# Kernel tuning notes

Measured on AMD Instinct MI355X. Metric: run time of the kernel, lower is better.

## Reference

```python
import jax, jax.numpy as jnp
import numpy as np

D_CONV = 4  # matches Mamba(d_conv=4)


def _silu(v):
    return v * jax.nn.sigmoid(v)


def _mamba_block(x, in_w, cw, cb, xw, dtw, dtb, A_log, Dp, ow):
    # x: (B, L, d_model)
    B, L, _ = x.shape
    d_inner, d_state = A_log.shape
    xz = x @ in_w.T                        # (B, L, 2*d_inner)
    xr, z = jnp.split(xz, 2, axis=-1)      # each (B, L, d_inner)
    # causal depthwise conv1d (pad d_conv-1 on the left, truncate to L)
    xp = jnp.pad(xr, ((0, 0), (D_CONV - 1, 0), (0, 0)))
    xc = sum(xp[:, k:k + L, :] * cw[:, k] for k in range(D_CONV)) + cb
    xc = _silu(xc)                         # (B, L, d_inner)
    dbl = xc @ xw.T                        # (B, L, dt_rank + 2*d_state)
    dt_rank = dbl.shape[-1] - 2 * d_state
    dt, Bm, Cm = jnp.split(dbl, [dt_rank, dt_rank + d_state], axis=-1)
    dt = jax.nn.softplus(dt @ dtw.T + dtb)  # (B, L, d_inner)
    A = -jnp.exp(A_log)                    # (d_inner, d_state)
    dA = jnp.exp(dt[..., None] * A)                          # (B, L, d_inner, d_state)
    dBx = dt[..., None] * Bm[:, :, None, :] * xc[..., None]  # (B, L, d_inner, d_state)

    def step(h, inputs):
        dA_t, dBx_t, C_t = inputs          # (B,d,s), (B,d,s), (B,s)
        h = dA_t * h + dBx_t
        y = jnp.einsum('bds,bs->bd', h, C_t)
        return h, y

    h0 = jnp.zeros((B, d_inner, d_state), x.dtype)
    _, ys = jax.lax.scan(step, h0, (dA.transpose(1, 0, 2, 3),
                                    dBx.transpose(1, 0, 2, 3),
                                    Cm.transpose(1, 0, 2)))
    y = ys.transpose(1, 0, 2) + xc * Dp    # skip term D*u
    y = y * _silu(z)                       # gated
    return y @ ow.T                        # (B, L, d_model)


def setup_inputs() -> dict:
    key = jax.random.key(0)
    d_model, d_state, n_layer = 1024, 16, 2
    d_inner = 2 * d_model
    dt_rank = d_model // 16  # ceil(1024/16)
    Bsz, L = 2, 1024
    ks = jax.random.split(key, 8)
    s = 0.02
    x = jax.random.normal(ks[0], (Bsz, L, d_model), jnp.float32)
    in_proj_w = jax.random.normal(ks[1], (n_layer, 2 * d_inner, d_model), jnp.float32) * s
    conv_w = jax.random.normal(ks[2], (n_layer, d_inner, D_CONV), jnp.float32) * 0.2
    conv_b = jnp.zeros((n_layer, d_inner), jnp.float32)
    x_proj_w = jax.random.normal(ks[3], (n_layer, dt_rank + 2 * d_state, d_inner), jnp.float32) * s
    dt_proj_w = jax.random.normal(ks[4], (n_layer, d_inner, dt_rank), jnp.float32) * s
    dt_proj_b = jax.random.uniform(ks[5], (n_layer, d_inner), jnp.float32, -5.0, -3.0)
    A_log = jnp.log(jnp.tile(jnp.arange(1, d_state + 1, dtype=jnp.float32), (n_layer, d_inner, 1)))
    D = jnp.ones((n_layer, d_inner), jnp.float32)
    out_proj_w = jax.random.normal(ks[6], (n_layer, d_model, d_inner), jnp.float32) * s
    return {"x": x, "in_proj_w": in_proj_w, "conv_w": conv_w, "conv_b": conv_b,
            "x_proj_w": x_proj_w, "dt_proj_w": dt_proj_w, "dt_proj_b": dt_proj_b,
            "A_log": A_log, "D": D, "out_proj_w": out_proj_w}


def reference(x, in_proj_w, conv_w, conv_b, x_proj_w, dt_proj_w, dt_proj_b, A_log, D, out_proj_w):
    n_layer = in_proj_w.shape[0]
    for i in range(n_layer):
        x = _mamba_block(x, in_proj_w[i], conv_w[i], conv_b[i], x_proj_w[i],
                         dt_proj_w[i], dt_proj_b[i], A_log[i], D[i], out_proj_w[i])
    return x
```

## Files before the change

kernel.cpp:

```cpp
#include <hip/hip_runtime.h>
#include <hip/hip_bf16.h>
#include <cmath>

typedef __bf16 bf16x8_t __attribute__((ext_vector_type(8)));
typedef float  f32x4_t  __attribute__((ext_vector_type(4)));
using bf16 = __hip_bfloat16;

#define LOG2E 1.44269504088896340736f
#define LN2   0.69314718055994530942f

#define AS1C(p) ((const __attribute__((address_space(1))) void*)(p))
#define AS3C(p) ((__attribute__((address_space(3))) void*)(p))

__device__ __forceinline__ float fexp2(float x) { return __builtin_amdgcn_exp2f(x); }
__device__ __forceinline__ float flog2(float x) { return __builtin_amdgcn_logf(x); }
__device__ __forceinline__ float frcp (float x) { return __builtin_amdgcn_rcpf(x); }

__global__ __launch_bounds__(256)
void cast_multi(const float* s0, bf16* d0, int e0,
                const float* s1, bf16* d1, int e1,
                const float* s2, bf16* d2, int e2,
                const float* s3, bf16* d3, int e3,
                const float* s4, bf16* d4, int e4)
{
    const int blk = blockIdx.x;
    const float* src; bf16* dst; int base;
    if      (blk < e0) { src = s0; dst = d0; base = blk; }
    else if (blk < e1) { src = s1; dst = d1; base = blk - e0; }
    else if (blk < e2) { src = s2; dst = d2; base = blk - e1; }
    else if (blk < e3) { src = s3; dst = d3; base = blk - e2; }
    else               { src = s4; dst = d4; base = blk - e3; }

    const int i = base * 256 + threadIdx.x;
    const float4* s = (const float4*)(src + (size_t)i * 8);
    float4 a = s[0], b = s[1];
    bf16 o[8];
    o[0] = __float2bfloat16(a.x); o[1] = __float2bfloat16(a.y);
    o[2] = __float2bfloat16(a.z); o[3] = __float2bfloat16(a.w);
    o[4] = __float2bfloat16(b.x); o[5] = __float2bfloat16(b.y);
    o[6] = __float2bfloat16(b.z); o[7] = __float2bfloat16(b.w);
    *(int4*)(dst + (size_t)i * 8) = *(int4*)o;
}

template<int MODE, bool SPLITK>
__global__ __launch_bounds__(256)
void gemm_bf16(const bf16* __restrict__ A, const bf16* __restrict__ B,
               float* __restrict__ Cf, bf16* __restrict__ Cb,
               int M, int N, int K, int lda, int ldb, int ldc)
{
    __shared__ __align__(16) bf16 At[2][64][32];
    __shared__ __align__(16) bf16 Bt[2][128][32];

    const int tid  = threadIdx.x;
    const int lane = tid & 63;
    const int wid  = tid >> 6;
    const int wr2  = wid & 1;
    const int wc2  = wid >> 1;
    const int fr   = lane & 15;
    const int fq   = lane >> 4;

    const int row0 = blockIdx.y * 64;
    const int col0 = blockIdx.x * 128;
    const int kb   = SPLITK ? blockIdx.z * K : 0;

    const int gA_row = wid * 16 + (lane >> 2);
    const int gB_row = wid * 32 + (lane >> 2);
    const int g_kp   = (((lane & 3) ^ ((lane >> 3) & 3)) * 8);
    const bf16* aP0 = A + (size_t)(row0 + gA_row) * lda + g_kp + kb;
    int bR0 = col0 + gB_row;      if (bR0 >= N) bR0 = N - 1;
    int bR1 = col0 + gB_row + 16; if (bR1 >= N) bR1 = N - 1;
    const bf16* bP0 = B + (size_t)bR0 * ldb + g_kp + kb;
    const bf16* bP1 = B + (size_t)bR1 * ldb + g_kp + kb;

    const int rchunk = (fq ^ ((fr >> 1) & 3)) * 8;

    f32x4_t acc[2][4];
    #pragma unroll
    for (int m = 0; m < 2; ++m)
        #pragma unroll
        for (int n = 0; n < 4; ++n)
            acc[m][n] = f32x4_t{0.f, 0.f, 0.f, 0.f};

    auto STAGE = [&](int buf, int k0) {
        __builtin_amdgcn_global_load_lds(AS1C(aP0 + k0), AS3C(&At[buf][wid * 16][0]),      16, 0, 0);
        __builtin_amdgcn_global_load_lds(AS1C(bP0 + k0), AS3C(&Bt[buf][wid * 32][0]),      16, 0, 0);
        __builtin_amdgcn_global_load_lds(AS1C(bP1 + k0), AS3C(&Bt[buf][wid * 32 + 16][0]), 16, 0, 0);
    };

    STAGE(0, 0);
    __syncthreads();
    int cur = 0;
    for (int k0 = 0; k0 < K; k0 += 32) {
        if (k0 + 32 < K) STAGE(cur ^ 1, k0 + 32);

        bf16x8_t af[2], bg[4];
        #pragma unroll
        for (int m = 0; m < 2; ++m)
            af[m] = *(const bf16x8_t*)&At[cur][wr2 * 32 + m * 16 + fr][rchunk];
        #pragma unroll
        for (int n = 0; n < 4; ++n)
            bg[n] = *(const bf16x8_t*)&Bt[cur][wc2 * 64 + n * 16 + fr][rchunk];
        #pragma unroll
        for (int m = 0; m < 2; ++m)
            #pragma unroll
            for (int n = 0; n < 4; ++n)
                acc[m][n] = __builtin_amdgcn_mfma_f32_16x16x32_bf16(
                    af[m], bg[n], acc[m][n], 0, 0, 0);

        __syncthreads();
        cur ^= 1;
    }

    float* Cfz = SPLITK ? (Cf + (size_t)blockIdx.z * M * ldc) : Cf;

    #pragma unroll
    for (int m = 0; m < 2; ++m) {
        #pragma unroll
        for (int n = 0; n < 4; ++n) {
            const int c = col0 + wc2 * 64 + n * 16 + fr;
            if (c < N) {
                #pragma unroll
                for (int r = 0; r < 4; ++r) {
                    const int rr = row0 + wr2 * 32 + m * 16 + fq * 4 + r;
                    if (SPLITK || MODE != 1) Cfz[(size_t)rr * ldc + c] = acc[m][n][r];
                    if (!SPLITK && MODE != 0) Cb[(size_t)rr * ldc + c] = __float2bfloat16(acc[m][n][r]);
                }
            }
        }
    }
}

__global__ __launch_bounds__(256)
void reduce_pk(const float* __restrict__ part, float* __restrict__ of,
               bf16* __restrict__ oh, int n4, int stride4, int S)
{
    const int i = blockIdx.x * blockDim.x + threadIdx.x;
    if (i >= n4) return;
    const float4* p4 = (const float4*)part;
    float4 s = p4[i];
    for (int k = 1; k < S; ++k) {
        float4 v = p4[(size_t)k * stride4 + i];
        s.x += v.x; s.y += v.y; s.z += v.z; s.w += v.w;
    }
    if (of) ((float4*)of)[i] = s;
    if (oh) {
        bf16 o[4];
        o[0] = __float2bfloat16(s.x); o[1] = __float2bfloat16(s.y);
        o[2] = __float2bfloat16(s.z); o[3] = __float2bfloat16(s.w);
        *(int2*)(oh + (size_t)i * 4) = *(int2*)o;
    }
}

__global__ __launch_bounds__(256)
void conv_silu(const bf16* __restrict__ xz, const float* __restrict__ cw,
               const float* __restrict__ cb, bf16* __restrict__ xc,
               int Bsz, int L, int dinner)
{
    const int nv = dinner / 4;
    const int L4 = L / 4;
    const int g  = blockIdx.x * blockDim.x + threadIdx.x;
    const int d4 = (g % nv) * 4;
    const int t4 = (g / nv) % L4;
    const int b  = g / (nv * L4);
    if (b >= Bsz) return;

    const int t0 = t4 * 4;
    const int ldxz = 2 * dinner;

    float4 w0 = *(const float4*)(cw + (size_t)(d4 + 0) * 4);
    float4 w1 = *(const float4*)(cw + (size_t)(d4 + 1) * 4);
    float4 w2 = *(const float4*)(cw + (size_t)(d4 + 2) * 4);
    float4 w3 = *(const float4*)(cw + (size_t)(d4 + 3) * 4);
    float4 bias = *(const float4*)(cb + d4);

    float4 r[7];
    const bf16* base = xz + (size_t)b * L * ldxz + d4;
    #pragma unroll
    for (int k = 0; k < 7; ++k) {
        const int ts = t0 - 3 + k;
        if (ts >= 0 && ts < L) {
            const bf16* rp = base + (size_t)ts * ldxz;
            r[k] = make_float4(__bfloat162float(rp[0]), __bfloat162float(rp[1]),
                               __bfloat162float(rp[2]), __bfloat162float(rp[3]));
        } else {
            r[k] = make_float4(0.f, 0.f, 0.f, 0.f);
        }
    }

    bf16* outp = xc + ((size_t)b * L + t0) * dinner + d4;
    #pragma unroll
    for (int j = 0; j < 4; ++j) {
        float4 acc = bias;
        #pragma unroll
        for (int k = 0; k < 4; ++k) {
            const float4 v = r[j + k];
            acc.x = fmaf(v.x, (&w0.x)[k], acc.x);
            acc.y = fmaf(v.y, (&w1.x)[k], acc.y);
            acc.z = fmaf(v.z, (&w2.x)[k], acc.z);
            acc.w = fmaf(v.w, (&w3.x)[k], acc.w);
        }
        acc.x = acc.x * frcp(1.f + fexp2(-acc.x * LOG2E));
        acc.y = acc.y * frcp(1.f + fexp2(-acc.y * LOG2E));
        acc.z = acc.z * frcp(1.f + fexp2(-acc.z * LOG2E));
        acc.w = acc.w * frcp(1.f + fexp2(-acc.w * LOG2E));
        bf16 o[4];
        o[0] = __float2bfloat16(acc.x); o[1] = __float2bfloat16(acc.y);
        o[2] = __float2bfloat16(acc.z); o[3] = __float2bfloat16(acc.w);
        *(int2*)(outp + (size_t)j * dinner) = *(int2*)o;
    }
}

__global__ __launch_bounds__(256)
void scan_part1(const bf16* __restrict__ dtraw, const bf16* __restrict__ xc,
                const float* __restrict__ dbl, const float* __restrict__ dtb,
                const float* __restrict__ alog, float* __restrict__ hend,
                float* __restrict__ Ssum, int Bsz, int L, int dinner,
                int NC, int CL)
{
    const int g  = blockIdx.x * blockDim.x + threadIdx.x;
    const int s8 = g & 1;
    const int d  = (g >> 1) % dinner;
    const int c  = ((g >> 1) / dinner) % NC;
    const int b  = g / (2 * dinner * NC);
    if (b >= Bsz) return;

    const float* ap = alog + (size_t)d * 16 + s8 * 8;
    float a_[8];
    *(float4*)&a_[0] = *(const float4*)(ap + 0);
    *(float4*)&a_[4] = *(const float4*)(ap + 4);
    float As[8];
    #pragma unroll
    for (int i = 0; i < 8; ++i) As[i] = -fexp2(a_[i] * LOG2E) * LOG2E;
    const float bias = dtb[d];

    const int t0 = c * CL;
    const bf16*  dt_p = dtraw + ((size_t)b * L + t0) * dinner + d;
    const bf16*  xc_p = xc    + ((size_t)b * L + t0) * dinner + d;
    const float* bl_p = dbl   + ((size_t)b * L + t0) * 96 + 64 + s8 * 8;

    float h[8];
    #pragma unroll
    for (int i = 0; i < 8; ++i) h[i] = 0.f;
    float S = 0.f;

    for (int t = 0; t < CL; ++t) {
        const float dtv = __bfloat162float(*dt_p);
        const float xcv = __bfloat162float(*xc_p);
        float Bv[8];
        *(float4*)&Bv[0] = *(const float4*)(bl_p + 0);
        *(float4*)&Bv[4] = *(const float4*)(bl_p + 4);

        const float xv = dtv + bias;
        const float e  = fexp2(xv * LOG2E);
        const float sp = (xv > 15.f) ? xv : LN2 * flog2(1.f + e);
        S += sp;
        const float u = sp * xcv;
        #pragma unroll
        for (int i = 0; i < 8; ++i)
            h[i] = fmaf(fexp2(sp * As[i]), h[i], u * Bv[i]);

        dt_p += dinner; xc_p += dinner; bl_p += 96;
    }

    const size_t idx = ((size_t)b * NC + c) * dinner + d;
    float* hp = hend + idx * 16 + s8 * 8;
    *(float4*)(hp + 0) = make_float4(h[0], h[1], h[2], h[3]);
    *(float4*)(hp + 4) = make_float4(h[4], h[5], h[6], h[7]);
    if (s8 == 0) Ssum[idx] = S;
}

__global__ __launch_bounds__(256)
void chunk_prefix(float* __restrict__ hend, const float* __restrict__ Ssum,
                  const float* __restrict__ alog, int Bsz, int dinner, int NC)
{
    const int g = blockIdx.x * blockDim.x + threadIdx.x;
    const int s = g & 15;
    const int d = (g >> 4) % dinner;
    const int b = g / (16 * dinner);
    if (b >= Bsz) return;

    const float As2 = -fexp2(alog[(size_t)d * 16 + s] * LOG2E) * LOG2E;

    size_t idx = (size_t)b * NC * dinner + d;
    float he = hend[idx * 16 + s];
    float Sv = Ssum[idx];
    float h = 0.f;
    for (int c = 0; c < NC; ++c) {
        float heN = 0.f, SvN = 0.f;
        if (c + 1 < NC) {
            heN = hend[(idx + dinner) * 16 + s];
            SvN = Ssum[idx + dinner];
        }
        hend[idx * 16 + s] = h;
        h = fmaf(fexp2(As2 * Sv), h, he);
        he = heN; Sv = SvN; idx += dinner;
    }
}

__global__ __launch_bounds__(256)
void scan_part2(bf16* dty, const bf16* __restrict__ xc,
                const float* __restrict__ dbl, const bf16* __restrict__ xz,
                const float* __restrict__ dtb, const float* __restrict__ alog,
                const float* __restrict__ Dp, const float* __restrict__ hinit,
                int Bsz, int L, int dinner, int NC, int CL)
{
    const int g  = blockIdx.x * blockDim.x + threadIdx.x;
    const int s8 = g & 1;
    const int d  = (g >> 1) % dinner;
    const int c  = ((g >> 1) / dinner) % NC;
    const int b  = g / (2 * dinner * NC);
    if (b >= Bsz) return;

    const float* ap = alog + (size_t)d * 16 + s8 * 8;
    float a_[8];
    *(float4*)&a_[0] = *(const float4*)(ap + 0);
    *(float4*)&a_[4] = *(const float4*)(ap + 4);
    float As[8];
    #pragma unroll
    for (int i = 0; i < 8; ++i) As[i] = -fexp2(a_[i] * LOG2E) * LOG2E;
    const float bias = dtb[d];
    const float Dval = Dp[d];

    const size_t cidx = ((size_t)b * NC + c) * dinner + d;
    float h[8];
    const float* hp = hinit + cidx * 16 + s8 * 8;
    *(float4*)&h[0] = *(const float4*)(hp + 0);
    *(float4*)&h[4] = *(const float4*)(hp + 4);

    const int t0 = c * CL;
    bf16*        dt_p = dty + ((size_t)b * L + t0) * dinner + d;
    const bf16*  xc_p = xc  + ((size_t)b * L + t0) * dinner + d;
    const float* bl_p = dbl + ((size_t)b * L + t0) * 96 + 64 + s8 * 8;
    const bf16*  z_p  = xz  + ((size_t)b * L + t0) * (2 * dinner) + dinner + d;

    for (int t = 0; t < CL; ++t) {
        const float dtv = __bfloat162float(*dt_p);
        const float xcv = __bfloat162float(*xc_p);
        const float zv  = __bfloat162float(*z_p);
        float Bv[8], Cv[8];
        *(float4*)&Bv[0] = *(const float4*)(bl_p + 0);
        *(float4*)&Bv[4] = *(const float4*)(bl_p + 4);
        *(float4*)&Cv[0] = *(const float4*)(bl_p + 16);
        *(float4*)&Cv[4] = *(const float4*)(bl_p + 20);

        const float xv = dtv + bias;
        const float e  = fexp2(xv * LOG2E);
        const float sp = (xv > 15.f) ? xv : LN2 * flog2(1.f + e);
        const float u = sp * xcv;
        float y = 0.f;
        #pragma unroll
        for (int i = 0; i < 8; ++i) {
            h[i] = fmaf(fexp2(sp * As[i]), h[i], u * Bv[i]);
            y = fmaf(h[i], Cv[i], y);
        }
        y += __shfl_xor(y, 1);

        if (s8 == 0) {
            y = fmaf(xcv, Dval, y);
            const float sig = frcp(1.f + fexp2(-zv * LOG2E));
            *dt_p = __float2bfloat16(y * (zv * sig));
        }

        dt_p += dinner; xc_p += dinner; bl_p += 96; z_p += 2 * dinner;
    }
}

extern "C" void kernel_launch(void* const* d_in, const int* in_sizes, int n_in,
                              void* d_out, int out_size, void* d_ws, size_t ws_size,
                              hipStream_t stream)
{
    const float* x    = (const float*)d_in[0];
    const float* inw  = (const float*)d_in[1];
    const float* cw   = (const float*)d_in[2];
    const float* cb   = (const float*)d_in[3];
    const float* xw   = (const float*)d_in[4];
    const float* dtw  = (const float*)d_in[5];
    const float* dtb  = (const float*)d_in[6];
    const float* alog = (const float*)d_in[7];
    const float* Dp   = (const float*)d_in[8];
    const float* ow   = (const float*)d_in[9];
    float* out = (float*)d_out;

    const int Bsz = 2, L = 1024, dmodel = 1024, dinner = 2048;
    const int BL = Bsz * L;
    const int NC = 64, CL = L / NC;
    const int SPX = 16, KSX = dinner / SPX;
    const int SPO = 2,  KSO = dinner / SPO;

    char* p = (char*)d_ws;
    auto alloc = [&](size_t bytes) { char* r = p; p += (bytes + 63) & ~size_t(63); return r; };
    bf16*  wb_in  = (bf16*) alloc((size_t)2 * 2 * dinner * dmodel * 2);
    bf16*  wb_x   = (bf16*) alloc((size_t)2 * 96 * dinner * 2);
    bf16*  wb_dt  = (bf16*) alloc((size_t)2 * dinner * 64 * 2);
    bf16*  wb_ow  = (bf16*) alloc((size_t)2 * dmodel * dinner * 2);
    bf16*  curb   = (bf16*) alloc((size_t)BL * dmodel * 2);
    bf16*  xzb16  = (bf16*) alloc((size_t)BL * 2 * dinner * 2);
    bf16*  xcb16  = (bf16*) alloc((size_t)BL * dinner * 2);
    float* dblb   = (float*)alloc((size_t)BL * 96 * 4);
    bf16*  dblb16 = (bf16*) alloc((size_t)BL * 96 * 2);
    bf16*  dtrb16 = (bf16*) alloc((size_t)BL * dinner * 2);
    float* ssumb  = (float*)alloc((size_t)Bsz * NC * dinner * 4);
    float* partb  = (float*)alloc((size_t)SPO * BL * dmodel * 4);
    float* hendb  = partb;

    const int scan_blocks = (Bsz * NC * dinner * 2) / 256;
    const int pfx_blocks  = (Bsz * dinner * 16) / 256;

    {
        const int n8_x  = BL * dmodel / 8;
        const int n8_in = 2 * 2 * dinner * dmodel / 8;
        const int n8_xw = 2 * 96 * dinner / 8;
        const int n8_dt = 2 * dinner * 64 / 8;
        const int n8_ow = 2 * dmodel * dinner / 8;
        const int e0 = n8_x / 256;
        const int e1 = e0 + n8_in / 256;
        const int e2 = e1 + n8_xw / 256;
        const int e3 = e2 + n8_dt / 256;
        const int e4 = e3 + n8_ow / 256;
        cast_multi<<<e4, 256, 0, stream>>>(
            x, curb, e0, inw, wb_in, e1, xw, wb_x, e2, dtw, wb_dt, e3, ow, wb_ow, e4);
    }

    for (int l = 0; l < 2; ++l) {
        const bf16*  wb_in_l = wb_in + (size_t)l * 2 * dinner * dmodel;
        const bf16*  wb_x_l  = wb_x  + (size_t)l * 96 * dinner;
        const bf16*  wb_dt_l = wb_dt + (size_t)l * dinner * 64;
        const bf16*  wb_ow_l = wb_ow + (size_t)l * dmodel * dinner;
        const float* cw_l    = cw   + (size_t)l * dinner * 4;
        const float* cb_l    = cb   + (size_t)l * dinner;
        const float* dtb_l   = dtb  + (size_t)l * dinner;
        const float* alog_l  = alog + (size_t)l * dinner * 16;
        const float* Dp_l    = Dp   + (size_t)l * dinner;

        gemm_bf16<1, false><<<dim3(2 * dinner / 128, BL / 64), 256, 0, stream>>>(
            curb, wb_in_l, nullptr, xzb16, BL, 2 * dinner, dmodel, dmodel, dmodel, 2 * dinner);

        conv_silu<<<(Bsz * (L / 4) * (dinner / 4)) / 256, 256, 0, stream>>>(
            xzb16, cw_l, cb_l, xcb16, Bsz, L, dinner);

        gemm_bf16<0, true><<<dim3(1, BL / 64, SPX), 256, 0, stream>>>(
            xcb16, wb_x_l, partb, nullptr, BL, 96, KSX, dinner, dinner, 96);
        reduce_pk<<<(BL * 96 / 4 + 255) / 256, 256, 0, stream>>>(
            partb, dblb, dblb16, BL * 96 / 4, BL * 96 / 4, SPX);

        gemm_bf16<1, false><<<dim3(dinner / 128, BL / 64), 256, 0, stream>>>(
            dblb16, wb_dt_l, nullptr, dtrb16, BL, dinner, 64, 96, 64, dinner);

        scan_part1<<<scan_blocks, 256, 0, stream>>>(
            dtrb16, xcb16, dblb, dtb_l, alog_l, hendb, ssumb, Bsz, L, dinner, NC, CL);
        chunk_prefix<<<pfx_blocks, 256, 0, stream>>>(
            hendb, ssumb, alog_l, Bsz, dinner, NC);
        scan_part2<<<scan_blocks, 256, 0, stream>>>(
            dtrb16, xcb16, dblb, xzb16, dtb_l, alog_l, Dp_l, hendb,
            Bsz, L, dinner, NC, CL);

        gemm_bf16<0, true><<<dim3(dmodel / 128, BL / 64, SPO), 256, 0, stream>>>(
            dtrb16, wb_ow_l, partb, nullptr, BL, dmodel, KSO, dinner, dinner, dmodel);
        if (l == 0)
            reduce_pk<<<(BL * dmodel / 4 + 255) / 256, 256, 0, stream>>>(
                partb, nullptr, curb, BL * dmodel / 4, BL * dmodel / 4, SPO);
        else
            reduce_pk<<<(BL * dmodel / 4 + 255) / 256, 256, 0, stream>>>(
                partb, out, nullptr, BL * dmodel / 4, BL * dmodel / 4, SPO);
    }
}
```

Before: 303.3 us.

## Deepen GEMM K tile to 64 and store scan chunk states in bf16

The bf16 MFMA GEMM now stages 64-wide K slices instead of 32. It uses a new XOR swizzle over two 32-element halves and issues two MFMA passes per tile, which halves the number of barrier and loop iterations. The chunked selective-scan intermediate states (hend) are written, prefixed and read back in bf16 rather than fp32, cutting the traffic between scan_part1, chunk_prefix and scan_part2. The trade-offs are double the LDS use per GEMM block, which may lower occupancy, and reduced precision on the carried recurrent state.

```diff
diff --git a/kernel.cpp b/kernel.cpp
--- a/kernel.cpp
+++ b/kernel.cpp
@@ -48,8 +48,8 @@
                float* __restrict__ Cf, bf16* __restrict__ Cb,
                int M, int N, int K, int lda, int ldb, int ldc)
 {
-    __shared__ __align__(16) bf16 At[2][64][32];
-    __shared__ __align__(16) bf16 Bt[2][128][32];
+    __shared__ __align__(16) bf16 At[2][64][64];
+    __shared__ __align__(16) bf16 Bt[2][128][64];
 
     const int tid  = threadIdx.x;
     const int lane = tid & 63;
@@ -63,16 +63,32 @@
     const int col0 = blockIdx.x * 128;
     const int kb   = SPLITK ? blockIdx.z * K : 0;
 
-    const int gA_row = wid * 16 + (lane >> 2);
-    const int gB_row = wid * 32 + (lane >> 2);
-    const int g_kp   = (((lane & 3) ^ ((lane >> 3) & 3)) * 8);
-    const bf16* aP0 = A + (size_t)(row0 + gA_row) * lda + g_kp + kb;
-    int bR0 = col0 + gB_row;      if (bR0 >= N) bR0 = N - 1;
-    int bR1 = col0 + gB_row + 16; if (bR1 >= N) bR1 = N - 1;
-    const bf16* bP0 = B + (size_t)bR0 * ldb + g_kp + kb;
-    const bf16* bP1 = B + (size_t)bR1 * ldb + g_kp + kb;
+    const int lr = lane >> 3;
+    const int lh = (lane >> 2) & 1;
+    const int lc = lane & 3;
+
+    auto srcA = [&](int rb) {
+        const int row = rb + lr;
+        const int k = ((lh ^ (row & 1)) * 32) + ((lc ^ ((row >> 1) & 3)) * 8);
+        return A + (size_t)(row0 + row) * lda + k + kb;
+    };
+    auto srcB = [&](int rb) {
+        const int row = rb + lr;
+        int gr = col0 + row; if (gr >= N) gr = N - 1;
+        const int k = ((lh ^ (row & 1)) * 32) + ((lc ^ ((row >> 1) & 3)) * 8);
+        return B + (size_t)gr * ldb + k + kb;
+    };
+    const bf16* aS0 = srcA(wid * 16);
+    const bf16* aS1 = srcA(wid * 16 + 8);
+    const bf16* bS0 = srcB(wid * 32);
+    const bf16* bS1 = srcB(wid * 32 + 8);
+    const bf16* bS2 = srcB(wid * 32 + 16);
+    const bf16* bS3 = srcB(wid * 32 + 24);
 
     const int rchunk = (fq ^ ((fr >> 1) & 3)) * 8;
+    const int rpar   = fr & 1;
+    const int off0   = (rpar)     * 32 + rchunk;
+    const int off1   = (rpar ^ 1) * 32 + rchunk;
 
     f32x4_t acc[2][4];
     #pragma unroll
@@ -82,30 +98,43 @@
             acc[m][n] = f32x4_t{0.f, 0.f, 0.f, 0.f};
 
     auto STAGE = [&](int buf, int k0) {
-        __builtin_amdgcn_global_load_lds(AS1C(aP0 + k0), AS3C(&At[buf][wid * 16][0]),      16, 0, 0);
-        __builtin_amdgcn_global_load_lds(AS1C(bP0 + k0), AS3C(&Bt[buf][wid * 32][0]),      16, 0, 0);
-        __builtin_amdgcn_global_load_lds(AS1C(bP1 + k0), AS3C(&Bt[buf][wid * 32 + 16][0]), 16, 0, 0);
+        __builtin_amdgcn_global_load_lds(AS1C(aS0 + k0), AS3C(&At[buf][wid * 16][0]),      16, 0, 0);
+        __builtin_amdgcn_global_load_lds(AS1C(aS1 + k0), AS3C(&At[buf][wid * 16 + 8][0]),  16, 0, 0);
+        __builtin_amdgcn_global_load_lds(AS1C(bS0 + k0), AS3C(&Bt[buf][wid * 32][0]),      16, 0, 0);
+        __builtin_amdgcn_global_load_lds(AS1C(bS1 + k0), AS3C(&Bt[buf][wid * 32 + 8][0]),  16, 0, 0);
+        __builtin_amdgcn_global_load_lds(AS1C(bS2 + k0), AS3C(&Bt[buf][wid * 32 + 16][0]), 16, 0, 0);
+        __builtin_amdgcn_global_load_lds(AS1C(bS3 + k0), AS3C(&Bt[buf][wid * 32 + 24][0]), 16, 0, 0);
     };
 
     STAGE(0, 0);
     __syncthreads();
     int cur = 0;
-    for (int k0 = 0; k0 < K; k0 += 32) {
-        if (k0 + 32 < K) STAGE(cur ^ 1, k0 + 32);
-
-        bf16x8_t af[2], bg[4];
-        #pragma unroll
-        for (int m = 0; m < 2; ++m)
-            af[m] = *(const bf16x8_t*)&At[cur][wr2 * 32 + m * 16 + fr][rchunk];
-        #pragma unroll
-        for (int n = 0; n < 4; ++n)
-            bg[n] = *(const bf16x8_t*)&Bt[cur][wc2 * 64 + n * 16 + fr][rchunk];
+    for (int k0 = 0; k0 < K; k0 += 64) {
+        if (k0 + 64 < K) STAGE(cur ^ 1, k0 + 64);
+
+        bf16x8_t af0[2], af1[2], bg0[4], bg1[4];
+        #pragma unroll
+        for (int m = 0; m < 2; ++m) {
+            af0[m] = *(const bf16x8_t*)&At[cur][wr2 * 32 + m * 16 + fr][off0];
+            af1[m] = *(const bf16x8_t*)&At[cur][wr2 * 32 + m * 16 + fr][off1];
+        }
+        #pragma unroll
+        for (int n = 0; n < 4; ++n) {
+            bg0[n] = *(const bf16x8_t*)&Bt[cur][wc2 * 64 + n * 16 + fr][off0];
+            bg1[n] = *(const bf16x8_t*)&Bt[cur][wc2 * 64 + n * 16 + fr][off1];
+        }
         #pragma unroll
         for (int m = 0; m < 2; ++m)
             #pragma unroll
             for (int n = 0; n < 4; ++n)
                 acc[m][n] = __builtin_amdgcn_mfma_f32_16x16x32_bf16(
-                    af[m], bg[n], acc[m][n], 0, 0, 0);
+                    af0[m], bg0[n], acc[m][n], 0, 0, 0);
+        #pragma unroll
+        for (int m = 0; m < 2; ++m)
+            #pragma unroll
+            for (int n = 0; n < 4; ++n)
+                acc[m][n] = __builtin_amdgcn_mfma_f32_16x16x32_bf16(
+                    af1[m], bg1[n], acc[m][n], 0, 0, 0);
 
         __syncthreads();
         cur ^= 1;
@@ -213,7 +242,7 @@
 __global__ __launch_bounds__(256)
 void scan_part1(const bf16* __restrict__ dtraw, const bf16* __restrict__ xc,
                 const float* __restrict__ dbl, const float* __restrict__ dtb,
-                const float* __restrict__ alog, float* __restrict__ hend,
+                const float* __restrict__ alog, bf16* __restrict__ hend,
                 float* __restrict__ Ssum, int Bsz, int L, int dinner,
                 int NC, int CL)
 {
@@ -263,14 +292,15 @@
     }
 
     const size_t idx = ((size_t)b * NC + c) * dinner + d;
-    float* hp = hend + idx * 16 + s8 * 8;
-    *(float4*)(hp + 0) = make_float4(h[0], h[1], h[2], h[3]);
-    *(float4*)(hp + 4) = make_float4(h[4], h[5], h[6], h[7]);
+    bf16 ho[8];
+    #pragma unroll
+    for (int i = 0; i < 8; ++i) ho[i] = __float2bfloat16(h[i]);
+    *(int4*)(hend + idx * 16 + s8 * 8) = *(int4*)ho;
     if (s8 == 0) Ssum[idx] = S;
 }
 
 __global__ __launch_bounds__(256)
-void chunk_prefix(float* __restrict__ hend, const float* __restrict__ Ssum,
+void chunk_prefix(bf16* __restrict__ hend, const float* __restrict__ Ssum,
                   const float* __restrict__ alog, int Bsz, int dinner, int NC)
 {
     const int g = blockIdx.x * blockDim.x + threadIdx.x;
@@ -282,16 +312,16 @@
     const float As2 = -fexp2(alog[(size_t)d * 16 + s] * LOG2E) * LOG2E;
 
     size_t idx = (size_t)b * NC * dinner + d;
-    float he = hend[idx * 16 + s];
+    float he = __bfloat162float(hend[idx * 16 + s]);
     float Sv = Ssum[idx];
     float h = 0.f;
     for (int c = 0; c < NC; ++c) {
         float heN = 0.f, SvN = 0.f;
         if (c + 1 < NC) {
-            heN = hend[(idx + dinner) * 16 + s];
+            heN = __bfloat162float(hend[(idx + dinner) * 16 + s]);
             SvN = Ssum[idx + dinner];
         }
-        hend[idx * 16 + s] = h;
+        hend[idx * 16 + s] = __float2bfloat16(h);
         h = fmaf(fexp2(As2 * Sv), h, he);
         he = heN; Sv = SvN; idx += dinner;
     }
@@ -301,7 +331,7 @@
 void scan_part2(bf16* dty, const bf16* __restrict__ xc,
                 const float* __restrict__ dbl, const bf16* __restrict__ xz,
                 const float* __restrict__ dtb, const float* __restrict__ alog,
-                const float* __restrict__ Dp, const float* __restrict__ hinit,
+                const float* __restrict__ Dp, const bf16* __restrict__ hinit,
                 int Bsz, int L, int dinner, int NC, int CL)
 {
     const int g  = blockIdx.x * blockDim.x + threadIdx.x;
@@ -322,10 +352,11 @@
     const float Dval = Dp[d];
 
     const size_t cidx = ((size_t)b * NC + c) * dinner + d;
+    bf16 hi[8];
+    *(int4*)hi = *(const int4*)(hinit + cidx * 16 + s8 * 8);
     float h[8];
-    const float* hp = hinit + cidx * 16 + s8 * 8;
-    *(float4*)&h[0] = *(const float4*)(hp + 0);
-    *(float4*)&h[4] = *(const float4*)(hp + 4);
+    #pragma unroll
+    for (int i = 0; i < 8; ++i) h[i] = __bfloat162float(hi[i]);
 
     const int t0 = c * CL;
     bf16*        dt_p = dty + ((size_t)b * L + t0) * dinner + d;
@@ -401,7 +432,7 @@
     bf16*  dtrb16 = (bf16*) alloc((size_t)BL * dinner * 2);
     float* ssumb  = (float*)alloc((size_t)Bsz * NC * dinner * 4);
     float* partb  = (float*)alloc((size_t)SPO * BL * dmodel * 4);
-    float* hendb  = partb;
+    bf16*  hendb  = (bf16*)partb;
 
     const int scan_blocks = (Bsz * NC * dinner * 2) / 256;
     const int pfx_blocks  = (Bsz * dinner * 16) / 256;
```

After: 305.1 us. About the same (+0.6%).
